# Optimization experiments

Measured on AMD Instinct MI355X. Metric: run time of the kernel, lower is better.

The kernel has to match this reference:

```python
import jax, jax.numpy as jnp
import numpy as np

N = 100000      # nodes
E = 1250000     # edges
DIN = 128       # input_feature_dim
H = 64          # hidden_feature_dim
C = 16          # num_classes
BN_EPS = 1e-5


def _linear_init(key, fin, fout):
    # torch.nn.Linear default: U(-1/sqrt(fin), 1/sqrt(fin)); stored as [fin, fout] for x @ W
    s = 1.0 / np.sqrt(fin)
    kw, kb = jax.random.split(key)
    w = jax.random.uniform(kw, (fin, fout), jnp.float32, -s, s)
    b = jax.random.uniform(kb, (fout,), jnp.float32, -s, s)
    return w, b


def setup_inputs() -> dict:
    key = jax.random.key(0)
    ks = jax.random.split(key, 16)
    inp = {}
    inp["x"] = jax.random.normal(ks[0], (N, DIN), jnp.float32)
    src = jax.random.randint(ks[1], (E,), 0, N)
    dst = jax.random.randint(ks[2], (E,), 0, N)
    inp["edge_index"] = jnp.stack([src, dst]).astype(jnp.int64)
    inp["fc1_w"], inp["fc1_b"] = _linear_init(ks[3], DIN, H)
    dims = [(H, H), (H, H), (H, C)]
    for i, (fi, fo) in enumerate(dims):
        w, b = _linear_init(ks[4 + i], fi, fo)
        inp[f"conv{i}_w"] = w
        inp[f"conv{i}_b"] = b
        inp[f"bn{i}_g"] = jnp.ones((fo,), jnp.float32)
        inp[f"bn{i}_b"] = jnp.zeros((fo,), jnp.float32)
    inp["fc2_w"], inp["fc2_b"] = _linear_init(ks[7], C, C)
    return inp


def gcn_conv(h, w, b, src, dst, n):
    # PyG GCNConv: linear transform, add self-loops, symmetric normalization,
    # scatter-add messages from src into dst, then add bias.
    h = h @ w                                   # [N, out]
    loops = jnp.arange(n)
    s = jnp.concatenate([src, loops])           # [E+N]
    d = jnp.concatenate([dst, loops])
    deg = jax.ops.segment_sum(jnp.ones(s.shape[0], h.dtype), d, num_segments=n)
    dinv = jnp.where(deg > 0, jax.lax.rsqrt(deg), 0.0)
    norm = dinv[s] * dinv[d]                    # [E+N]
    msg = h[s] * norm[:, None]                  # [E+N, out] gather + scale
    out = jax.ops.segment_sum(msg, d, num_segments=n)
    return out + b


def batch_norm(x, gamma, beta):
    # BatchNorm1d in training mode: biased batch statistics over nodes
    mu = x.mean(axis=0)
    var = x.var(axis=0)
    return (x - mu) * jax.lax.rsqrt(var + BN_EPS) * gamma + beta


def reference(x, edge_index, fc1_w, fc1_b,
              conv0_w, conv0_b, bn0_g, bn0_b,
              conv1_w, conv1_b, bn1_g, bn1_b,
              conv2_w, conv2_b, bn2_g, bn2_b,
              fc2_w, fc2_b):
    src, dst = edge_index[0], edge_index[1]
    n = x.shape[0]
    h = jax.nn.relu(x @ fc1_w + fc1_b)
    layers = [(conv0_w, conv0_b, bn0_g, bn0_b),
              (conv1_w, conv1_b, bn1_g, bn1_b),
              (conv2_w, conv2_b, bn2_g, bn2_b)]
    for w, b, g, be in layers:
        h = jax.nn.relu(batch_norm(gcn_conv(h, w, b, src, dst, n), g, be))
    h = h @ fc2_w + fc2_b
    return jax.nn.log_softmax(h, axis=1)
```

## Files before the change

### kernel.cpp

```cpp
#include <hip/hip_runtime.h>

#define BN_EPS 1e-5f

typedef unsigned int uint32;

__device__ __forceinline__ void fma4(float4& a, float s, const float4& w) {
    a.x = fmaf(s, w.x, a.x); a.y = fmaf(s, w.y, a.y);
    a.z = fmaf(s, w.z, a.z); a.w = fmaf(s, w.w, a.w);
}

__device__ __forceinline__ float blo(uint32 p) { return __uint_as_float(p << 16); }
__device__ __forceinline__ float bhi(uint32 p) { return __uint_as_float(p & 0xFFFF0000u); }
__device__ __forceinline__ uint32 f2bf1(float f) {
    uint32 u = __float_as_uint(f);
    return (u + 0x7FFFu + ((u >> 16) & 1u)) >> 16;
}
__device__ __forceinline__ uint32 packbf(float a, float b) { return f2bf1(a) | (f2bf1(b) << 16); }


__global__ __launch_bounds__(256) void k_deg_count(const int* __restrict__ dst, int* deg, int e) {
    int i = blockIdx.x * 256 + threadIdx.x;
    if (i < e) atomicAdd(&deg[dst[i]], 1);
}


__global__ __launch_bounds__(256) void k_scan1(const int* __restrict__ deg, int* __restrict__ off,
                                               int* __restrict__ bsum, float* __restrict__ dinv, int n) {
    __shared__ int sh[256];
    int i = blockIdx.x * 256 + threadIdx.x;
    int v = (i < n) ? deg[i] : 0;
    if (i < n) dinv[i] = rsqrtf((float)v + 1.0f);
    sh[threadIdx.x] = v;
    __syncthreads();
    #pragma unroll
    for (int d = 1; d < 256; d <<= 1) {
        int t = (threadIdx.x >= d) ? sh[threadIdx.x - d] : 0;
        __syncthreads();
        sh[threadIdx.x] += t;
        __syncthreads();
    }
    if (i < n) off[i] = sh[threadIdx.x] - v;
    if (threadIdx.x == 255) bsum[blockIdx.x] = sh[255];
}

__global__ __launch_bounds__(512) void k_scan2(int* bsum, int nb) {
    __shared__ int sh[512];
    int v = (threadIdx.x < nb) ? bsum[threadIdx.x] : 0;
    sh[threadIdx.x] = v;
    __syncthreads();
    #pragma unroll
    for (int d = 1; d < 512; d <<= 1) {
        int t = (threadIdx.x >= d) ? sh[threadIdx.x - d] : 0;
        __syncthreads();
        sh[threadIdx.x] += t;
        __syncthreads();
    }
    if (threadIdx.x < nb) bsum[threadIdx.x] = sh[threadIdx.x] - v;
}

__global__ __launch_bounds__(256) void k_scan3(int* __restrict__ off, const int* __restrict__ bsum,
                                               int* __restrict__ cnt, int n, int e) {
    int i = blockIdx.x * 256 + threadIdx.x;
    if (i < n) { off[i] += bsum[blockIdx.x]; cnt[i] = 0; }
    if (i == 0) off[n] = e;
}

__global__ __launch_bounds__(256) void k_fill(const int* __restrict__ src, const int* __restrict__ dst,
                                              const int* __restrict__ off, int* __restrict__ cnt,
                                              int* __restrict__ esrc, int e) {
    int i = blockIdx.x * 256 + threadIdx.x;
    if (i < e) {
        int d = dst[i];
        int slot = off[d] + atomicAdd(&cnt[d], 1);
        esrc[slot] = src[i];
    }
}


template<int FIN, int FOUT, bool RELU, bool BIAS, bool BNIN, bool DSCALE, bool OBF>
__global__ __launch_bounds__(256) void k_linear(const float* __restrict__ X, const float* __restrict__ W,
                                                const float* __restrict__ bias, void* __restrict__ Yv,
                                                const float* __restrict__ S, const float* __restrict__ bng,
                                                const float* __restrict__ bnb, const float* __restrict__ dinv,
                                                float inv_n, int n) {
    constexpr int KC = 64;
    constexpr int TX = FOUT / 4;
    constexpr int TY = 256 / TX;
    constexpr int RQ = (FOUT == 64) ? 8 : 2;
    constexpr int TILE_R = TY * RQ;
    constexpr int LDX = KC + 4;
    constexpr int LDW = FOUT + 4;
    __shared__ float Xs[TILE_R][LDX];
    __shared__ float Ws[KC][LDW];
    __shared__ float scs[BNIN ? FIN : 4], sfs[BNIN ? FIN : 4];

    const int tx = threadIdx.x % TX;
    const int ty = threadIdx.x / TX;

    if (BNIN) {
        for (int c = threadIdx.x; c < FIN; c += 256) {
            float mu = S[c] * inv_n;
            float var = S[FIN + c] * inv_n - mu * mu;
            float is = rsqrtf(var + BN_EPS) * bng[c];
            scs[c] = is;
            sfs[c] = bnb[c] - mu * is;
        }
        __syncthreads();
    }

    float4 bb = make_float4(0.f, 0.f, 0.f, 0.f);
    if (BIAS) bb = *(const float4*)(bias + tx * 4);

    for (int r0 = blockIdx.x * TILE_R; r0 < n; r0 += gridDim.x * TILE_R) {
        float4 acc[RQ];
        #pragma unroll
        for (int q = 0; q < RQ; ++q) acc[q] = bb;

        for (int kc = 0; kc < FIN; kc += KC) {
            __syncthreads();
            for (int idx = threadIdx.x; idx < TILE_R * (KC / 4); idx += 256) {
                int rr = idx / (KC / 4), k4 = idx % (KC / 4);
                int row = r0 + rr;
                float4 v = make_float4(0.f, 0.f, 0.f, 0.f);
                if (row < n) v = *(const float4*)(X + (size_t)row * FIN + kc + 4 * k4);
                if (BNIN) {
                    int c = kc + 4 * k4;
                    v.x = fmaxf(fmaf(v.x, scs[c+0], sfs[c+0]), 0.f);
                    v.y = fmaxf(fmaf(v.y, scs[c+1], sfs[c+1]), 0.f);
                    v.z = fmaxf(fmaf(v.z, scs[c+2], sfs[c+2]), 0.f);
                    v.w = fmaxf(fmaf(v.w, scs[c+3], sfs[c+3]), 0.f);
                }
                *(float4*)(&Xs[rr][4 * k4]) = v;
            }
            for (int idx = threadIdx.x; idx < KC * (FOUT / 4); idx += 256) {
                int kk = idx / (FOUT / 4), c4 = idx % (FOUT / 4);
                *(float4*)(&Ws[kk][4 * c4]) = *(const float4*)(W + (size_t)(kc + kk) * FOUT + 4 * c4);
            }
            __syncthreads();

            #pragma unroll 4
            for (int k4 = 0; k4 < KC / 4; ++k4) {
                float4 w0 = *(const float4*)(&Ws[4*k4+0][tx*4]);
                float4 w1 = *(const float4*)(&Ws[4*k4+1][tx*4]);
                float4 w2 = *(const float4*)(&Ws[4*k4+2][tx*4]);
                float4 w3 = *(const float4*)(&Ws[4*k4+3][tx*4]);
                #pragma unroll
                for (int q = 0; q < RQ; ++q) {
                    float4 xv = *(const float4*)(&Xs[ty*RQ+q][4*k4]);
                    fma4(acc[q], xv.x, w0);
                    fma4(acc[q], xv.y, w1);
                    fma4(acc[q], xv.z, w2);
                    fma4(acc[q], xv.w, w3);
                }
            }
        }

        #pragma unroll
        for (int q = 0; q < RQ; ++q) {
            int row = r0 + ty * RQ + q;
            if (row < n) {
                float4 v = acc[q];
                if (RELU) {
                    v.x = fmaxf(v.x, 0.f); v.y = fmaxf(v.y, 0.f);
                    v.z = fmaxf(v.z, 0.f); v.w = fmaxf(v.w, 0.f);
                }
                if (DSCALE) {
                    float dv = dinv[row];
                    v.x *= dv; v.y *= dv; v.z *= dv; v.w *= dv;
                }
                if (OBF) {
                    uint2 pk;
                    pk.x = packbf(v.x, v.y);
                    pk.y = packbf(v.z, v.w);
                    ((uint2*)Yv)[(size_t)row * (FOUT / 4) + tx] = pk;
                } else {
                    *(float4*)((float*)Yv + (size_t)row * FOUT + tx * 4) = v;
                }
            }
        }
    }
}


__global__ __launch_bounds__(256) void k_accum64bf(const uint32* __restrict__ Tb, const int* __restrict__ esrc,
                                                   const int* __restrict__ off, const float* __restrict__ dinv,
                                                   const float* __restrict__ bias, float* __restrict__ Z,
                                                   float* __restrict__ S, int n, int e) {
    __shared__ uint32 ring[4][2][256];
    __shared__ float sA[4][64], sB[4][64];

    const int lane = threadIdx.x & 63;
    const int wid  = threadIdx.x >> 6;
    const int rsub = lane >> 3;
    const int csub = lane & 7;
    const int cidx = lane >> 1;
    const int chal = lane & 1;
    const float bcol = bias[lane];

    float s1 = 0.f, s2 = 0.f;

    const int gw = blockIdx.x * 4 + wid;
    const int NW = gridDim.x * 4;
    const int eS = (int)((long long)gw * e / NW);
    const int eE = (int)((long long)(gw + 1) * e / NW);

    int lo = 0, hi = n;
    while (lo < hi) { int mid = (lo + hi) >> 1; if (off[mid] < eS) lo = mid + 1; else hi = mid; }
    const int d0 = lo;
    int d1;
    if (gw == NW - 1) d1 = n;
    else {
        lo = d0; hi = n;
        while (lo < hi) { int mid = (lo + hi) >> 1; if (off[mid] < eE) lo = mid + 1; else hi = mid; }
        d1 = lo;
    }

    if (d0 < d1) {
        const int e0 = off[d0];
        const int e1 = off[d1];
        const int nt = (e1 - e0 + 7) >> 3;

        uint32* slot0 = &ring[wid][0][0];
        uint32* slot1 = &ring[wid][1][0];

        int d = d0;
        int nxt = off[d + 1];
        uint32 selfp = Tb[(size_t)d * 32 + cidx];
        float  dv    = dinv[d];
        float  part  = 0.f;
        int    ec    = e0;

        auto tload = [&](int t) -> uint4 {
            int ei = min(e0 + t * 8 + rsub, e1 - 1);
            int s = esrc[ei];
            return ((const uint4*)Tb)[(size_t)s * 8 + csub];
        };

        uint4 B0, B1, B2;
        if (nt > 0) B0 = tload(0);
        if (nt > 1) B1 = tload(1);
        if (nt > 2) B2 = tload(2);

        for (int t = 0; t < nt; ++t) {
            uint32* sl = (t & 1) ? slot1 : slot0;
            uint4 cur = (t % 3 == 0) ? B0 : (t % 3 == 1) ? B1 : B2;
            *(uint4*)(sl + lane * 4) = cur;
            if (t + 3 < nt) {
                if (t % 3 == 0) B0 = tload(t + 3);
                else if (t % 3 == 1) B1 = tload(t + 3);
                else B2 = tload(t + 3);
            }
            int rend = min(8, e1 - (e0 + t * 8));
            for (int r = 0; r < rend; ++r) {
                while (ec == nxt) {
                    float sv = chal ? bhi(selfp) : blo(selfp);
                    float z = fmaf(part + sv, dv, bcol);
                    Z[(size_t)d * 64 + lane] = z;
                    s1 += z; s2 += z * z;
                    part = 0.f;
                    ++d;
                    nxt = off[d + 1];
                    selfp = Tb[(size_t)d * 32 + cidx];
                    dv = dinv[d];
                }
                uint32 p = sl[r * 32 + cidx];
                part += chal ? bhi(p) : blo(p);
                ++ec;
            }
        }
        while (d < d1) {
            float sv = chal ? bhi(selfp) : blo(selfp);
            float z = fmaf(part + sv, dv, bcol);
            Z[(size_t)d * 64 + lane] = z;
            s1 += z; s2 += z * z;
            part = 0.f;
            ++d;
            if (d < d1) {
                selfp = Tb[(size_t)d * 32 + cidx];
                dv = dinv[d];
            }
        }
    }

    sA[wid][lane] = s1;
    sB[wid][lane] = s2;
    __syncthreads();
    if (threadIdx.x < 64) {
        float t1 = 0.f, t2 = 0.f;
        #pragma unroll
        for (int w = 0; w < 4; ++w) { t1 += sA[w][threadIdx.x]; t2 += sB[w][threadIdx.x]; }
        atomicAdd(&S[threadIdx.x], t1);
        atomicAdd(&S[64 + threadIdx.x], t2);
    }
}


__global__ __launch_bounds__(256) void k_accum16bf(const uint2* __restrict__ Tb2, const int* __restrict__ esrc,
                                                   const int* __restrict__ off, const float* __restrict__ dinv,
                                                   const float* __restrict__ bias, float* __restrict__ Z,
                                                   float* __restrict__ S, int n) {
    const int lane = threadIdx.x & 63;
    const int wid  = threadIdx.x >> 6;
    const int lp   = lane & 3;
    const int es   = lane >> 2;
    const float4 bb = *(const float4*)(bias + 4 * lp);
    float st1[4] = {0.f,0.f,0.f,0.f}, st2[4] = {0.f,0.f,0.f,0.f};
    const uint2 z2 = make_uint2(0u, 0u);

    for (int dp = blockIdx.x * 4 + wid; 2 * dp < n; dp += gridDim.x * 4) {
        const int dA = 2 * dp, dB = 2 * dp + 1;
        const int oA0 = off[dA], oA1 = off[dA + 1];
        const int oB0 = oA1;
        const int oB1 = (dB < n) ? off[dB + 1] : oA1;

        float aA0=0.f, aA1=0.f, aA2=0.f, aA3=0.f;
        float aB0=0.f, aB1=0.f, aB2=0.f, aB3=0.f;
        int bA = oA0, bB = oB0;
        while (bA < oA1 || bB < oB1) {
            if (bA < oA1) {
                int i0 = bA + es;
                int s0 = (i0 < oA1) ? esrc[i0] : -1;
                uint2 p0 = (s0 >= 0) ? Tb2[(size_t)s0 * 4 + lp] : z2;
                aA0 += blo(p0.x); aA1 += bhi(p0.x); aA2 += blo(p0.y); aA3 += bhi(p0.y);
            }
            if (bB < oB1) {
                int i0 = bB + es;
                int s0 = (i0 < oB1) ? esrc[i0] : -1;
                uint2 p0 = (s0 >= 0) ? Tb2[(size_t)s0 * 4 + lp] : z2;
                aB0 += blo(p0.x); aB1 += bhi(p0.x); aB2 += blo(p0.y); aB3 += bhi(p0.y);
            }
            bA += 16; bB += 16;
        }

        #pragma unroll
        for (int sh = 4; sh <= 32; sh <<= 1) {
            aA0 += __shfl_xor(aA0, sh); aA1 += __shfl_xor(aA1, sh);
            aA2 += __shfl_xor(aA2, sh); aA3 += __shfl_xor(aA3, sh);
            aB0 += __shfl_xor(aB0, sh); aB1 += __shfl_xor(aB1, sh);
            aB2 += __shfl_xor(aB2, sh); aB3 += __shfl_xor(aB3, sh);
        }

        if (es == 0) {
            uint2 ps = Tb2[(size_t)dA * 4 + lp];
            float dv = dinv[dA];
            float4 zz;
            zz.x = fmaf(aA0 + blo(ps.x), dv, bb.x);
            zz.y = fmaf(aA1 + bhi(ps.x), dv, bb.y);
            zz.z = fmaf(aA2 + blo(ps.y), dv, bb.z);
            zz.w = fmaf(aA3 + bhi(ps.y), dv, bb.w);
            *(float4*)(Z + (size_t)dA * 16 + 4 * lp) = zz;
            st1[0] += zz.x; st2[0] += zz.x * zz.x;
            st1[1] += zz.y; st2[1] += zz.y * zz.y;
            st1[2] += zz.z; st2[2] += zz.z * zz.z;
            st1[3] += zz.w; st2[3] += zz.w * zz.w;
            if (dB < n) {
                uint2 pb = Tb2[(size_t)dB * 4 + lp];
                float dvB = dinv[dB];
                float4 zb;
                zb.x = fmaf(aB0 + blo(pb.x), dvB, bb.x);
                zb.y = fmaf(aB1 + bhi(pb.x), dvB, bb.y);
                zb.z = fmaf(aB2 + blo(pb.y), dvB, bb.z);
                zb.w = fmaf(aB3 + bhi(pb.y), dvB, bb.w);
                *(float4*)(Z + (size_t)dB * 16 + 4 * lp) = zb;
                st1[0] += zb.x; st2[0] += zb.x * zb.x;
                st1[1] += zb.y; st2[1] += zb.y * zb.y;
                st1[2] += zb.z; st2[2] += zb.z * zb.z;
                st1[3] += zb.w; st2[3] += zb.w * zb.w;
            }
        }
    }

    __shared__ float sh1[4][16], sh2[4][16];
    if (es == 0) {
        *(float4*)(&sh1[wid][4 * lp]) = make_float4(st1[0], st1[1], st1[2], st1[3]);
        *(float4*)(&sh2[wid][4 * lp]) = make_float4(st2[0], st2[1], st2[2], st2[3]);
    }
    __syncthreads();
    if (threadIdx.x < 16) {
        float t1 = 0.f, t2 = 0.f;
        #pragma unroll
        for (int w = 0; w < 4; ++w) { t1 += sh1[w][threadIdx.x]; t2 += sh2[w][threadIdx.x]; }
        atomicAdd(&S[threadIdx.x], t1);
        atomicAdd(&S[16 + threadIdx.x], t2);
    }
}


__global__ __launch_bounds__(256) void k_fc2_lsm(const float* __restrict__ Hin, const float* __restrict__ W,
                                                 const float* __restrict__ bias, const float* __restrict__ S,
                                                 const float* __restrict__ bng, const float* __restrict__ bnb,
                                                 float inv_n, float* __restrict__ out, int n) {
    __shared__ float Ws[256];
    __shared__ float bs[16], sc[16], sf[16];
    Ws[threadIdx.x] = W[threadIdx.x];
    if (threadIdx.x < 16) {
        int c = threadIdx.x;
        bs[c] = bias[c];
        float mu = S[c] * inv_n;
        float var = S[16 + c] * inv_n - mu * mu;
        float is = rsqrtf(var + BN_EPS) * bng[c];
        sc[c] = is;
        sf[c] = bnb[c] - mu * is;
    }
    __syncthreads();
    for (int row = blockIdx.x * 256 + threadIdx.x; row < n; row += gridDim.x * 256) {
        float h[16];
        const float4* hp = (const float4*)(Hin + (size_t)row * 16);
        #pragma unroll
        for (int q = 0; q < 4; ++q) {
            float4 h4 = hp[q];
            h[q*4+0] = h4.x; h[q*4+1] = h4.y; h[q*4+2] = h4.z; h[q*4+3] = h4.w;
        }
        #pragma unroll
        for (int k = 0; k < 16; ++k) h[k] = fmaxf(fmaf(h[k], sc[k], sf[k]), 0.0f);
        float o[16];
        #pragma unroll
        for (int c = 0; c < 16; ++c) {
            float acc = bs[c];
            #pragma unroll
            for (int k = 0; k < 16; ++k) acc += h[k] * Ws[k * 16 + c];
            o[c] = acc;
        }
        float m = o[0];
        #pragma unroll
        for (int c = 1; c < 16; ++c) m = fmaxf(m, o[c]);
        float ssum = 0.f;
        #pragma unroll
        for (int c = 0; c < 16; ++c) ssum += expf(o[c] - m);
        float lse = m + logf(ssum);
        float4* op = (float4*)(out + (size_t)row * 16);
        #pragma unroll
        for (int q = 0; q < 4; ++q) {
            float4 w4;
            w4.x = o[q*4+0] - lse; w4.y = o[q*4+1] - lse;
            w4.z = o[q*4+2] - lse; w4.w = o[q*4+3] - lse;
            op[q] = w4;
        }
    }
}


extern "C" void kernel_launch(void* const* d_in, const int* in_sizes, int n_in,
                              void* d_out, int out_size, void* d_ws, size_t ws_size,
                              hipStream_t stream) {
    const float* x      = (const float*)d_in[0];
    const int*   ei     = (const int*)d_in[1];
    const float* fc1_w  = (const float*)d_in[2];
    const float* fc1_b  = (const float*)d_in[3];
    const float* conv_w[3] = { (const float*)d_in[4],  (const float*)d_in[8],  (const float*)d_in[12] };
    const float* conv_b[3] = { (const float*)d_in[5],  (const float*)d_in[9],  (const float*)d_in[13] };
    const float* bn_g[3]   = { (const float*)d_in[6],  (const float*)d_in[10], (const float*)d_in[14] };
    const float* bn_b[3]   = { (const float*)d_in[7],  (const float*)d_in[11], (const float*)d_in[15] };
    const float* fc2_w  = (const float*)d_in[16];
    const float* fc2_b  = (const float*)d_in[17];

    const int n = in_sizes[0] / 128;
    const int e = in_sizes[1] / 2;
    const int* src = ei;
    const int* dst = ei + e;
    const float inv_n = 1.0f / (float)n;

    float*  A    = (float*)d_ws;
    float*  Bf   = A + (size_t)n * 64;
    uint32* Bb   = (uint32*)Bf;
    uint2*  Bb2  = (uint2*)Bf;
    float*  dinv = Bf + (size_t)n * 64;
    int*    deg  = (int*)(dinv + n);
    float*  stats = (float*)(deg + n);
    int*    off  = (int*)(stats + 384);
    int*    esrc = off + n + 1;
    int*    bsum = esrc + e;

    const int gN  = (n + 255) / 256;
    const int gE  = (e + 255) / 256;
    const int gAcc = 2048;
    const int gLin = (n + 127) / 128;

    float* st[3] = { stats, stats + 128, stats + 256 };

    hipMemsetAsync(deg, 0, ((size_t)n + 384) * sizeof(int), stream);
    k_deg_count<<<gE, 256, 0, stream>>>(dst, deg, e);
    k_scan1<<<gN, 256, 0, stream>>>(deg, off, bsum, dinv, n);
    k_scan2<<<1, 512, 0, stream>>>(bsum, gN);
    k_scan3<<<gN, 256, 0, stream>>>(off, bsum, deg , n, e);
    k_fill<<<gE, 256, 0, stream>>>(src, dst, off, deg , esrc, e);

    k_linear<128, 64, true, true, false, false, false><<<gLin, 256, 0, stream>>>(
        x, fc1_w, fc1_b, A, nullptr, nullptr, nullptr, nullptr, 0.f, n);

    k_linear<64, 64, false, false, false, true, true><<<gLin, 256, 0, stream>>>(
        A, conv_w[0], nullptr, Bb, nullptr, nullptr, nullptr, dinv, 0.f, n);
    k_accum64bf<<<gAcc, 256, 0, stream>>>(Bb, esrc, off, dinv, conv_b[0], A, st[0], n, e);

    k_linear<64, 64, false, false, true, true, true><<<gLin, 256, 0, stream>>>(
        A, conv_w[1], nullptr, Bb, st[0], bn_g[0], bn_b[0], dinv, inv_n, n);
    k_accum64bf<<<gAcc, 256, 0, stream>>>(Bb, esrc, off, dinv, conv_b[1], A, st[1], n, e);

    k_linear<64, 16, false, false, true, true, true><<<gLin, 256, 0, stream>>>(
        A, conv_w[2], nullptr, Bb2, st[1], bn_g[1], bn_b[1], dinv, inv_n, n);
    k_accum16bf<<<gAcc, 256, 0, stream>>>(Bb2, esrc, off, dinv, conv_b[2], A, st[2], n);

    k_fc2_lsm<<<gLin, 256, 0, stream>>>(A, fc2_w, fc2_b, st[2], bn_g[2], bn_b[2], inv_n, (float*)d_out, n);
}
```

Before: 475.2 us.

## Co-schedule degree count with fc1 and CSR fill with conv0 linear in shared grids

Merges independent stages into single launches: one grid runs the fc1 linear on even blocks while the other blocks atomically count degrees, and a second grid runs the conv0 linear while the remaining blocks fill the CSR edge list. The aim is to overlap memory-bound atomic scatter work with compute-bound GEMM tiles and to drop launches. In exchange the GEMM blocks run on a grid-stride loop and block roles interleave. The conv0 linear now writes the bf16 output through a uint2 view of the same buffer.

```diff
diff --git a/kernel.cpp b/kernel.cpp
--- a/kernel.cpp
+++ b/kernel.cpp
@@ -16,12 +16,6 @@
     return (u + 0x7FFFu + ((u >> 16) & 1u)) >> 16;
 }
 __device__ __forceinline__ uint32 packbf(float a, float b) { return f2bf1(a) | (f2bf1(b) << 16); }
-
-
-__global__ __launch_bounds__(256) void k_deg_count(const int* __restrict__ dst, int* deg, int e) {
-    int i = blockIdx.x * 256 + threadIdx.x;
-    if (i < e) atomicAdd(&deg[dst[i]], 1);
-}
 
 
 __global__ __launch_bounds__(256) void k_scan1(const int* __restrict__ deg, int* __restrict__ off,
@@ -65,14 +59,161 @@
     if (i == 0) off[n] = e;
 }
 
-__global__ __launch_bounds__(256) void k_fill(const int* __restrict__ src, const int* __restrict__ dst,
-                                              const int* __restrict__ off, int* __restrict__ cnt,
-                                              int* __restrict__ esrc, int e) {
-    int i = blockIdx.x * 256 + threadIdx.x;
-    if (i < e) {
-        int d = dst[i];
-        int slot = off[d] + atomicAdd(&cnt[d], 1);
-        esrc[slot] = src[i];
+
+__global__ __launch_bounds__(256) void k_fc1_deg(const float* __restrict__ X, const float* __restrict__ W,
+                                                 const float* __restrict__ bias, float* __restrict__ Y,
+                                                 const int* __restrict__ dst, int* __restrict__ deg,
+                                                 int n, int e, int nbLin) {
+    constexpr int FIN = 128, FOUT = 64, KC = 64;
+    constexpr int TX = FOUT / 4, TY = 256 / TX, RQ = 8, TILE_R = TY * RQ;
+    __shared__ float Xs[TILE_R][KC + 4];
+    __shared__ float Ws[KC][FOUT + 4];
+
+    const int bid = blockIdx.x;
+    const int twice = 2 * nbLin;
+    bool isLin; int vid;
+    if (bid < twice) { isLin = ((bid & 1) == 0); vid = bid >> 1; }
+    else { isLin = false; vid = nbLin + (bid - twice); }
+
+    if (!isLin) {
+        const int ndeg = gridDim.x - nbLin;
+        for (size_t i = (size_t)vid * 256 + threadIdx.x; i < (size_t)e; i += (size_t)ndeg * 256)
+            atomicAdd(&deg[dst[i]], 1);
+        return;
+    }
+
+    const int tx = threadIdx.x % TX;
+    const int ty = threadIdx.x / TX;
+    const float4 bb = *(const float4*)(bias + tx * 4);
+
+    for (int r0 = vid * TILE_R; r0 < n; r0 += nbLin * TILE_R) {
+        float4 acc[RQ];
+        #pragma unroll
+        for (int q = 0; q < RQ; ++q) acc[q] = bb;
+
+        for (int kc = 0; kc < FIN; kc += KC) {
+            __syncthreads();
+            for (int idx = threadIdx.x; idx < TILE_R * (KC / 4); idx += 256) {
+                int rr = idx / (KC / 4), k4 = idx % (KC / 4);
+                int row = r0 + rr;
+                float4 v = make_float4(0.f, 0.f, 0.f, 0.f);
+                if (row < n) v = *(const float4*)(X + (size_t)row * FIN + kc + 4 * k4);
+                *(float4*)(&Xs[rr][4 * k4]) = v;
+            }
+            for (int idx = threadIdx.x; idx < KC * (FOUT / 4); idx += 256) {
+                int kk = idx / (FOUT / 4), c4 = idx % (FOUT / 4);
+                *(float4*)(&Ws[kk][4 * c4]) = *(const float4*)(W + (size_t)(kc + kk) * FOUT + 4 * c4);
+            }
+            __syncthreads();
+
+            #pragma unroll 4
+            for (int k4 = 0; k4 < KC / 4; ++k4) {
+                float4 w0 = *(const float4*)(&Ws[4*k4+0][tx*4]);
+                float4 w1 = *(const float4*)(&Ws[4*k4+1][tx*4]);
+                float4 w2 = *(const float4*)(&Ws[4*k4+2][tx*4]);
+                float4 w3 = *(const float4*)(&Ws[4*k4+3][tx*4]);
+                #pragma unroll
+                for (int q = 0; q < RQ; ++q) {
+                    float4 xv = *(const float4*)(&Xs[ty*RQ+q][4*k4]);
+                    fma4(acc[q], xv.x, w0);
+                    fma4(acc[q], xv.y, w1);
+                    fma4(acc[q], xv.z, w2);
+                    fma4(acc[q], xv.w, w3);
+                }
+            }
+        }
+
+        #pragma unroll
+        for (int q = 0; q < RQ; ++q) {
+            int row = r0 + ty * RQ + q;
+            if (row < n) {
+                float4 v = acc[q];
+                v.x = fmaxf(v.x, 0.f); v.y = fmaxf(v.y, 0.f);
+                v.z = fmaxf(v.z, 0.f); v.w = fmaxf(v.w, 0.f);
+                *(float4*)(Y + (size_t)row * FOUT + tx * 4) = v;
+            }
+        }
+    }
+}
+
+
+__global__ __launch_bounds__(256) void k_conv0_fill(const float* __restrict__ X, const float* __restrict__ W,
+                                                    uint2* __restrict__ Yb, const float* __restrict__ dinv,
+                                                    const int* __restrict__ src, const int* __restrict__ dst,
+                                                    const int* __restrict__ off, int* __restrict__ cnt,
+                                                    int* __restrict__ esrc, int n, int e, int nbLin) {
+    constexpr int FIN = 64, FOUT = 64, KC = 64;
+    constexpr int TX = FOUT / 4, TY = 256 / TX, RQ = 8, TILE_R = TY * RQ;
+    __shared__ float Xs[TILE_R][KC + 4];
+    __shared__ float Ws[KC][FOUT + 4];
+
+    const int bid = blockIdx.x;
+    const int twice = 2 * nbLin;
+    bool isLin; int vid;
+    if (bid < twice) { isLin = ((bid & 1) == 0); vid = bid >> 1; }
+    else { isLin = false; vid = nbLin + (bid - twice); }
+
+    if (!isLin) {
+        const int nfl = gridDim.x - nbLin;
+        for (size_t i = (size_t)vid * 256 + threadIdx.x; i < (size_t)e; i += (size_t)nfl * 256) {
+            int d = dst[i];
+            int slot = off[d] + atomicAdd(&cnt[d], 1);
+            esrc[slot] = src[i];
+        }
+        return;
+    }
+
+    const int tx = threadIdx.x % TX;
+    const int ty = threadIdx.x / TX;
+
+    for (int r0 = vid * TILE_R; r0 < n; r0 += nbLin * TILE_R) {
+        float4 acc[RQ];
+        #pragma unroll
+        for (int q = 0; q < RQ; ++q) acc[q] = make_float4(0.f, 0.f, 0.f, 0.f);
+
+        __syncthreads();
+        for (int idx = threadIdx.x; idx < TILE_R * (KC / 4); idx += 256) {
+            int rr = idx / (KC / 4), k4 = idx % (KC / 4);
+            int row = r0 + rr;
+            float4 v = make_float4(0.f, 0.f, 0.f, 0.f);
+            if (row < n) v = *(const float4*)(X + (size_t)row * FIN + 4 * k4);
+            *(float4*)(&Xs[rr][4 * k4]) = v;
+        }
+        for (int idx = threadIdx.x; idx < KC * (FOUT / 4); idx += 256) {
+            int kk = idx / (FOUT / 4), c4 = idx % (FOUT / 4);
+            *(float4*)(&Ws[kk][4 * c4]) = *(const float4*)(W + (size_t)kk * FOUT + 4 * c4);
+        }
+        __syncthreads();
+
+        #pragma unroll 4
+        for (int k4 = 0; k4 < KC / 4; ++k4) {
+            float4 w0 = *(const float4*)(&Ws[4*k4+0][tx*4]);
+            float4 w1 = *(const float4*)(&Ws[4*k4+1][tx*4]);
+            float4 w2 = *(const float4*)(&Ws[4*k4+2][tx*4]);
+            float4 w3 = *(const float4*)(&Ws[4*k4+3][tx*4]);
+            #pragma unroll
+            for (int q = 0; q < RQ; ++q) {
+                float4 xv = *(const float4*)(&Xs[ty*RQ+q][4*k4]);
+                fma4(acc[q], xv.x, w0);
+                fma4(acc[q], xv.y, w1);
+                fma4(acc[q], xv.z, w2);
+                fma4(acc[q], xv.w, w3);
+            }
+        }
+
+        #pragma unroll
+        for (int q = 0; q < RQ; ++q) {
+            int row = r0 + ty * RQ + q;
+            if (row < n) {
+                float4 v = acc[q];
+                float dv = dinv[row];
+                v.x *= dv; v.y *= dv; v.z *= dv; v.w *= dv;
+                uint2 pk;
+                pk.x = packbf(v.x, v.y);
+                pk.y = packbf(v.z, v.w);
+                Yb[(size_t)row * (FOUT / 4) + tx] = pk;
+            }
+        }
     }
 }
 
@@ -472,24 +613,22 @@
     int*    bsum = esrc + e;
 
     const int gN  = (n + 255) / 256;
-    const int gE  = (e + 255) / 256;
     const int gAcc = 2048;
     const int gLin = (n + 127) / 128;
+    const int nbLin = gLin;
+    const int gFused = 2048;
 
     float* st[3] = { stats, stats + 128, stats + 256 };
 
     hipMemsetAsync(deg, 0, ((size_t)n + 384) * sizeof(int), stream);
-    k_deg_count<<<gE, 256, 0, stream>>>(dst, deg, e);
+
+    k_fc1_deg<<<gFused, 256, 0, stream>>>(x, fc1_w, fc1_b, A, dst, deg, n, e, nbLin);
+
     k_scan1<<<gN, 256, 0, stream>>>(deg, off, bsum, dinv, n);
     k_scan2<<<1, 512, 0, stream>>>(bsum, gN);
     k_scan3<<<gN, 256, 0, stream>>>(off, bsum, deg , n, e);
-    k_fill<<<gE, 256, 0, stream>>>(src, dst, off, deg , esrc, e);
-
-    k_linear<128, 64, true, true, false, false, false><<<gLin, 256, 0, stream>>>(
-        x, fc1_w, fc1_b, A, nullptr, nullptr, nullptr, nullptr, 0.f, n);
-
-    k_linear<64, 64, false, false, false, true, true><<<gLin, 256, 0, stream>>>(
-        A, conv_w[0], nullptr, Bb, nullptr, nullptr, nullptr, dinv, 0.f, n);
+
+    k_conv0_fill<<<gFused, 256, 0, stream>>>(A, conv_w[0], Bb2, dinv, src, dst, off, deg , esrc, n, e, nbLin);
     k_accum64bf<<<gAcc, 256, 0, stream>>>(Bb, esrc, off, dinv, conv_b[0], A, st[0], n, e);
 
     k_linear<64, 64, false, false, true, true, true><<<gLin, 256, 0, stream>>>(
```

Measured after the change: 403.8 us, median of 2. 1.18x faster.
